# Performance work log

Measured on AMD Instinct MI355X. Metric: run time of the kernel, lower is better.

The kernel has to match this reference:

```python
import jax, jax.numpy as jnp
import numpy as np

B, D, L, E, R = 16384, 2048, 3, 8, 64


def setup_inputs() -> dict:
    key = jax.random.key(0)
    k1, k2, k3, k4 = jax.random.split(key, 4)
    scale = 1.0 / np.sqrt(D)  # ~ PyTorch Linear default init scale
    X0 = jax.random.normal(k1, (B, D), dtype=jnp.float32)
    U = jax.random.normal(k2, (L, E, R, D), dtype=jnp.float32) * scale
    V = jax.random.normal(k3, (L, E, R, D), dtype=jnp.float32) * scale
    Wg = jax.random.normal(k4, (L, E, D), dtype=jnp.float32) * scale
    bg = jnp.zeros((L, E), dtype=jnp.float32)
    return {"X0": X0, "U": U, "V": V, "Wg": Wg, "bg": bg}


def reference(X0, U, V, Wg, bg):
    # X0: (B, D); U, V: (L, E, R, D); Wg: (L, E, D); bg: (L, E)
    Xi = X0
    num_layers = U.shape[0]
    for l in range(num_layers):  # small fixed layer count
        gate = jax.nn.softmax(jnp.einsum('bd,ed->be', Xi, Wg[l]) + bg[l], axis=1)  # (B, E)
        Uo = jnp.einsum('bd,erd->ber', Xi, U[l])  # (B, E, R)
        Vo = jnp.einsum('bd,erd->ber', Xi, V[l])  # (B, E, R)
        expert_out = jnp.sum(Uo * Vo, axis=2)     # (B, E) low-rank bilinear forms
        xw = jnp.sum(expert_out * gate, axis=1, keepdims=True)  # (B, 1)
        Xi = Xi + X0 * xw  # residual cross update (dropout=0, eval mode)
    return Xi
```

## Files before the change

### kernel.cpp

```cpp
#include <hip/hip_runtime.h>
#include <hip/hip_bf16.h>

#define BDIM 16384
#define DDIM 2048
#define LNUM 3
#define ENUM 8
#define NP 24

#define BM 256
#define BK 32

typedef _Float16 f16x8 __attribute__((ext_vector_type(8)));
typedef _Float16 f16x4 __attribute__((ext_vector_type(4)));
typedef float f32x4 __attribute__((ext_vector_type(4)));

__global__ void cvt_w_kernel(const float* __restrict__ U, const float* __restrict__ V,
                             _Float16* __restrict__ Wh) {
    size_t f = (size_t)blockIdx.x * blockDim.x + threadIdx.x;
    size_t elem = f * 4;
    int d   = (int)(elem & (DDIM - 1));
    int row = (int)((elem >> 11) & 127);
    int p   = (int)(elem >> 18);
    const float* src = (row < 64)
        ? (U + ((size_t)(p * 64 + row) * DDIM + d))
        : (V + ((size_t)(p * 64 + (row - 64)) * DDIM + d));
    float4 v = *(const float4*)src;
    f16x4 h = { (_Float16)v.x, (_Float16)v.y, (_Float16)v.z, (_Float16)v.w };
    ((f16x4*)Wh)[f] = h;
}

__global__ __launch_bounds__(256, 4) void gate_kernel(
    const float* __restrict__ X0, const float* __restrict__ Wg,
    float* __restrict__ G, _Float16* __restrict__ X0h) {
    __shared__ float Wgs[NP * 256];
    const int tid = (int)threadIdx.x;
    const int rq  = tid >> 3;
    const int q   = tid & 7;
    const int r0  = blockIdx.x * 64 + rq;
    const int r1  = r0 + 32;

    float acc[2][NP];
#pragma unroll
    for (int r = 0; r < 2; ++r)
#pragma unroll
        for (int j = 0; j < NP; ++j) acc[r][j] = 0.f;

    const float4* x0p = (const float4*)(X0 + (size_t)r0 * DDIM);
    const float4* x1p = (const float4*)(X0 + (size_t)r1 * DDIM);
    f16x4* h0p = (f16x4*)(X0h + (size_t)r0 * DDIM);
    f16x4* h1p = (f16x4*)(X0h + (size_t)r1 * DDIM);

    for (int k0 = 0; k0 < DDIM; k0 += 256) {
        __syncthreads();
#pragma unroll
        for (int t = tid; t < NP * 64; t += 256)
            ((float4*)Wgs)[t] =
                ((const float4*)Wg)[(size_t)(t >> 6) * (DDIM / 4) + (k0 >> 2) + (t & 63)];
        __syncthreads();
#pragma unroll 2
        for (int i = 0; i < 8; ++i) {
            int f4 = i * 8 + q;
            int gc = (k0 >> 2) + f4;
            float4 x0 = x0p[gc];
            float4 x1 = x1p[gc];
            f16x4 h0 = { (_Float16)x0.x, (_Float16)x0.y, (_Float16)x0.z, (_Float16)x0.w };
            f16x4 h1 = { (_Float16)x1.x, (_Float16)x1.y, (_Float16)x1.z, (_Float16)x1.w };
            h0p[gc] = h0;
            h1p[gc] = h1;
#pragma unroll
            for (int j = 0; j < NP; ++j) {
                float4 w = ((const float4*)(Wgs + j * 256))[f4];
                acc[0][j] += x0.x * w.x + x0.y * w.y + x0.z * w.z + x0.w * w.w;
                acc[1][j] += x1.x * w.x + x1.y * w.y + x1.z * w.z + x1.w * w.w;
            }
        }
    }
#pragma unroll
    for (int r = 0; r < 2; ++r)
#pragma unroll
        for (int j = 0; j < NP; ++j) {
            float v = acc[r][j];
            v += __shfl_xor(v, 1);
            v += __shfl_xor(v, 2);
            v += __shfl_xor(v, 4);
            if (q == 0) G[(size_t)j * BDIM + (r == 0 ? r0 : r1)] = v;
        }
}

__global__ __launch_bounds__(256, 2) void gemm_t_kernel(
    const _Float16* __restrict__ Ah,
    const _Float16* __restrict__ Bh,
    float* __restrict__ T)
{
    const int p    = blockIdx.y;
    const int m0   = blockIdx.x * BM;
    const int tid  = (int)threadIdx.x;
    const int wave = tid >> 6;
    const int lane = tid & 63;
    const int mlane = lane & 15;
    const int quad  = lane >> 4;

    __shared__ _Float16 As[BM * BK];
    __shared__ _Float16 Bs[128 * BK];

    const _Float16* Bp = Bh + (size_t)p * 128 * DDIM;

    f32x4 acc[4][8];
#pragma unroll
    for (int i = 0; i < 4; ++i)
#pragma unroll
        for (int j = 0; j < 8; ++j) acc[i][j] = (f32x4){0.f, 0.f, 0.f, 0.f};

    const int srow = lane >> 2;
    const int scol = ((lane & 3) ^ ((lane >> 3) & 3)) * 8;
    const int sw   = (mlane >> 1) & 3;

    for (int k0 = 0; k0 < DDIM; k0 += BK) {
        __syncthreads();
#pragma unroll
        for (int q = 0; q < 4; ++q) {
            int r16 = wave * 64 + q * 16;
            const _Float16* ga = Ah + (size_t)(m0 + r16 + srow) * DDIM + k0 + scol;
            __builtin_amdgcn_global_load_lds(
                (const __attribute__((address_space(1))) void*)ga,
                (__attribute__((address_space(3))) void*)&As[r16 * BK], 16, 0, 0);
        }
#pragma unroll
        for (int q = 0; q < 2; ++q) {
            int r16 = wave * 32 + q * 16;
            const _Float16* gb = Bp + (size_t)(r16 + srow) * DDIM + k0 + scol;
            __builtin_amdgcn_global_load_lds(
                (const __attribute__((address_space(1))) void*)gb,
                (__attribute__((address_space(3))) void*)&Bs[r16 * BK], 16, 0, 0);
        }
        __syncthreads();

        f16x8 aF[4], bF[8];
#pragma unroll
        for (int mi = 0; mi < 4; ++mi)
            aF[mi] = *(const f16x8*)&As[(wave * 64 + mi * 16 + mlane) * BK + ((quad ^ sw) * 8)];
#pragma unroll
        for (int ni = 0; ni < 8; ++ni)
            bF[ni] = *(const f16x8*)&Bs[(ni * 16 + mlane) * BK + ((quad ^ sw) * 8)];
#pragma unroll
        for (int mi = 0; mi < 4; ++mi)
#pragma unroll
            for (int ni = 0; ni < 8; ++ni)
                acc[mi][ni] = __builtin_amdgcn_mfma_f32_16x16x32_f16(
                    aF[mi], bF[ni], acc[mi][ni], 0, 0, 0);
    }

#pragma unroll
    for (int mi = 0; mi < 4; ++mi) {
#pragma unroll
        for (int j = 0; j < 4; ++j) {
            float tp = 0.f;
#pragma unroll
            for (int ni = 0; ni < 4; ++ni)
                tp += acc[mi][ni][j] * acc[mi][ni + 4][j];
            tp += __shfl_xor(tp, 1);
            tp += __shfl_xor(tp, 2);
            tp += __shfl_xor(tp, 4);
            tp += __shfl_xor(tp, 8);
            if (mlane == 0) {
                int m = wave * 64 + mi * 16 + quad * 4 + j;
                T[(size_t)p * BDIM + (m0 + m)] = tp;
            }
        }
    }
}

__global__ void epilogue_kernel(const _Float16* __restrict__ X0h,
                                const float* __restrict__ T,
                                const float* __restrict__ G,
                                const float* __restrict__ bg,
                                float* __restrict__ out) {
    __shared__ float s_sh[16];
    const int b0 = blockIdx.x * 16;
    const int tid = (int)threadIdx.x;
    if (tid < 16) {
        int b = b0 + tid;
        float s = 1.f;
#pragma unroll
        for (int l = 0; l < LNUM; ++l) {
            float logit[ENUM];
            float mx = -1e30f;
#pragma unroll
            for (int e = 0; e < ENUM; ++e) {
                int j = l * ENUM + e;
                float g = s * G[(size_t)j * BDIM + b] + bg[j];
                logit[e] = g;
                mx = fmaxf(mx, g);
            }
            float den = 0.f, num = 0.f;
            float s2 = s * s;
#pragma unroll
            for (int e = 0; e < ENUM; ++e) {
                int j = l * ENUM + e;
                float w = __expf(logit[e] - mx);
                den += w;
                num += w * (s2 * T[(size_t)j * BDIM + b]);
            }
            s += num / den;
        }
        s_sh[tid] = s;
    }
    __syncthreads();
    const int nf4 = DDIM / 4;
    for (int idx = tid; idx < 16 * nf4; idx += 256) {
        int r = idx >> 9;
        int c = idx & (nf4 - 1);
        float s = s_sh[r];
        f16x4 h = ((const f16x4*)(X0h + (size_t)(b0 + r) * DDIM))[c];
        float4 x = { s * (float)h[0], s * (float)h[1], s * (float)h[2], s * (float)h[3] };
        ((float4*)(out + (size_t)(b0 + r) * DDIM))[c] = x;
    }
}

extern "C" void kernel_launch(void* const* d_in, const int* in_sizes, int n_in,
                              void* d_out, int out_size, void* d_ws, size_t ws_size,
                              hipStream_t stream) {
    const float* X0 = (const float*)d_in[0];
    const float* U  = (const float*)d_in[1];
    const float* V  = (const float*)d_in[2];
    const float* Wg = (const float*)d_in[3];
    const float* bg = (const float*)d_in[4];
    float* out = (float*)d_out;

    char* ws = (char*)d_ws;
    _Float16* X0h = (_Float16*)ws;
    _Float16* Wh  = (_Float16*)(ws + 67108864ull);
    float* T      = (float*)(ws + 67108864ull + 12582912ull);
    float* G      = (float*)(ws + 67108864ull + 12582912ull + 1572864ull);

    cvt_w_kernel<<<dim3((NP * 128 * DDIM / 4) / 256), dim3(256), 0, stream>>>(U, V, Wh);
    gate_kernel<<<dim3(BDIM / 64), dim3(256), 0, stream>>>(X0, Wg, G, X0h);
    gemm_t_kernel<<<dim3(BDIM / BM, NP), dim3(256), 0, stream>>>(X0h, Wh, T);
    epilogue_kernel<<<dim3(BDIM / 16), dim3(256), 0, stream>>>(X0h, T, G, bg, out);
}
```

Before: 537.1 us.

## Fold gate projection into the fp16 MFMA GEMM as an extra grid slice

Replaces the scalar fp32 gate kernel, which both converted X0 to fp16 and computed the 24 gate logits with FMAs, with a plain conversion kernel plus a 25th blockIdx.y slice of the MFMA GEMM. That slice multiplies the fp16 X0 by an fp16 copy of Wg and writes the gate logits directly. The aim is to remove the slow scalar dot-product pass in favour of tensor-core work that reuses the existing GEMM tiling. In exchange, gate logits are now computed in fp16 rather than fp32, the gate slice spends MFMA work on padded columns (rows past 24 are loads of duplicated rows), and two extra small kernel launches are added.

Result: faster. 524.1 us (-2.4%).

```diff
diff --git a/kernel.cpp b/kernel.cpp
--- a/kernel.cpp
+++ b/kernel.cpp
@@ -6,6 +6,7 @@
 #define LNUM 3
 #define ENUM 8
 #define NP 24
+#define NPG 25
 
 #define BM 256
 #define BK 32
@@ -29,68 +30,26 @@
     ((f16x4*)Wh)[f] = h;
 }
 
-__global__ __launch_bounds__(256, 4) void gate_kernel(
-    const float* __restrict__ X0, const float* __restrict__ Wg,
-    float* __restrict__ G, _Float16* __restrict__ X0h) {
-    __shared__ float Wgs[NP * 256];
-    const int tid = (int)threadIdx.x;
-    const int rq  = tid >> 3;
-    const int q   = tid & 7;
-    const int r0  = blockIdx.x * 64 + rq;
-    const int r1  = r0 + 32;
-
-    float acc[2][NP];
-#pragma unroll
-    for (int r = 0; r < 2; ++r)
-#pragma unroll
-        for (int j = 0; j < NP; ++j) acc[r][j] = 0.f;
-
-    const float4* x0p = (const float4*)(X0 + (size_t)r0 * DDIM);
-    const float4* x1p = (const float4*)(X0 + (size_t)r1 * DDIM);
-    f16x4* h0p = (f16x4*)(X0h + (size_t)r0 * DDIM);
-    f16x4* h1p = (f16x4*)(X0h + (size_t)r1 * DDIM);
-
-    for (int k0 = 0; k0 < DDIM; k0 += 256) {
-        __syncthreads();
-#pragma unroll
-        for (int t = tid; t < NP * 64; t += 256)
-            ((float4*)Wgs)[t] =
-                ((const float4*)Wg)[(size_t)(t >> 6) * (DDIM / 4) + (k0 >> 2) + (t & 63)];
-        __syncthreads();
-#pragma unroll 2
-        for (int i = 0; i < 8; ++i) {
-            int f4 = i * 8 + q;
-            int gc = (k0 >> 2) + f4;
-            float4 x0 = x0p[gc];
-            float4 x1 = x1p[gc];
-            f16x4 h0 = { (_Float16)x0.x, (_Float16)x0.y, (_Float16)x0.z, (_Float16)x0.w };
-            f16x4 h1 = { (_Float16)x1.x, (_Float16)x1.y, (_Float16)x1.z, (_Float16)x1.w };
-            h0p[gc] = h0;
-            h1p[gc] = h1;
-#pragma unroll
-            for (int j = 0; j < NP; ++j) {
-                float4 w = ((const float4*)(Wgs + j * 256))[f4];
-                acc[0][j] += x0.x * w.x + x0.y * w.y + x0.z * w.z + x0.w * w.w;
-                acc[1][j] += x1.x * w.x + x1.y * w.y + x1.z * w.z + x1.w * w.w;
-            }
-        }
-    }
-#pragma unroll
-    for (int r = 0; r < 2; ++r)
-#pragma unroll
-        for (int j = 0; j < NP; ++j) {
-            float v = acc[r][j];
-            v += __shfl_xor(v, 1);
-            v += __shfl_xor(v, 2);
-            v += __shfl_xor(v, 4);
-            if (q == 0) G[(size_t)j * BDIM + (r == 0 ? r0 : r1)] = v;
-        }
+__global__ void cvt_wg_kernel(const float* __restrict__ Wg, _Float16* __restrict__ Wgh) {
+    int f = (int)(blockIdx.x * blockDim.x + threadIdx.x);
+    float4 v = ((const float4*)Wg)[f];
+    f16x4 h = { (_Float16)v.x, (_Float16)v.y, (_Float16)v.z, (_Float16)v.w };
+    ((f16x4*)Wgh)[f] = h;
+}
+
+__global__ void cvt_x_kernel(const float* __restrict__ X0, _Float16* __restrict__ X0h) {
+    size_t f = (size_t)blockIdx.x * blockDim.x + threadIdx.x;
+    float4 v = ((const float4*)X0)[f];
+    f16x4 h = { (_Float16)v.x, (_Float16)v.y, (_Float16)v.z, (_Float16)v.w };
+    ((f16x4*)X0h)[f] = h;
 }
 
 __global__ __launch_bounds__(256, 2) void gemm_t_kernel(
     const _Float16* __restrict__ Ah,
     const _Float16* __restrict__ Bh,
-    float* __restrict__ T)
+    const _Float16* __restrict__ Wgh,
+    float* __restrict__ T,
+    float* __restrict__ G)
 {
     const int p    = blockIdx.y;
     const int m0   = blockIdx.x * BM;
@@ -103,8 +62,6 @@
     __shared__ _Float16 As[BM * BK];
     __shared__ _Float16 Bs[128 * BK];
 
-    const _Float16* Bp = Bh + (size_t)p * 128 * DDIM;
-
     f32x4 acc[4][8];
 #pragma unroll
     for (int i = 0; i < 4; ++i)
@@ -114,6 +71,9 @@
     const int srow = lane >> 2;
     const int scol = ((lane & 3) ^ ((lane >> 3) & 3)) * 8;
     const int sw   = (mlane >> 1) & 3;
+
+    const bool gate = (p == NP);
+    const _Float16* Bp = gate ? Wgh : (Bh + (size_t)p * 128 * DDIM);
 
     for (int k0 = 0; k0 < DDIM; k0 += BK) {
         __syncthreads();
@@ -128,7 +88,9 @@
 #pragma unroll
         for (int q = 0; q < 2; ++q) {
             int r16 = wave * 32 + q * 16;
-            const _Float16* gb = Bp + (size_t)(r16 + srow) * DDIM + k0 + scol;
+            int r   = r16 + srow;
+            int rb  = (gate && r >= NP) ? (r & 15) : r;
+            const _Float16* gb = Bp + (size_t)rb * DDIM + k0 + scol;
             __builtin_amdgcn_global_load_lds(
                 (const __attribute__((address_space(1))) void*)gb,
                 (__attribute__((address_space(3))) void*)&Bs[r16 * BK], 16, 0, 0);
@@ -150,23 +112,39 @@
                     aF[mi], bF[ni], acc[mi][ni], 0, 0, 0);
     }
 
-#pragma unroll
-    for (int mi = 0; mi < 4; ++mi) {
-#pragma unroll
-        for (int j = 0; j < 4; ++j) {
-            float tp = 0.f;
-#pragma unroll
-            for (int ni = 0; ni < 4; ++ni)
-                tp += acc[mi][ni][j] * acc[mi][ni + 4][j];
-            tp += __shfl_xor(tp, 1);
-            tp += __shfl_xor(tp, 2);
-            tp += __shfl_xor(tp, 4);
-            tp += __shfl_xor(tp, 8);
-            if (mlane == 0) {
-                int m = wave * 64 + mi * 16 + quad * 4 + j;
-                T[(size_t)p * BDIM + (m0 + m)] = tp;
-            }
-        }
+    if (!gate) {
+#pragma unroll
+        for (int mi = 0; mi < 4; ++mi) {
+#pragma unroll
+            for (int j = 0; j < 4; ++j) {
+                float tp = 0.f;
+#pragma unroll
+                for (int ni = 0; ni < 4; ++ni)
+                    tp += acc[mi][ni][j] * acc[mi][ni + 4][j];
+                tp += __shfl_xor(tp, 1);
+                tp += __shfl_xor(tp, 2);
+                tp += __shfl_xor(tp, 4);
+                tp += __shfl_xor(tp, 8);
+                if (mlane == 0) {
+                    int m = wave * 64 + mi * 16 + quad * 4 + j;
+                    T[(size_t)p * BDIM + (m0 + m)] = tp;
+                }
+            }
+        }
+    } else {
+#pragma unroll
+        for (int mi = 0; mi < 4; ++mi)
+#pragma unroll
+            for (int ni = 0; ni < 2; ++ni) {
+                int col = ni * 16 + mlane;
+                if (col < NP) {
+#pragma unroll
+                    for (int j = 0; j < 4; ++j) {
+                        int m = wave * 64 + mi * 16 + quad * 4 + j;
+                        G[(size_t)col * BDIM + (m0 + m)] = acc[mi][ni][j];
+                    }
+                }
+            }
     }
 }
 
@@ -230,11 +208,13 @@
     char* ws = (char*)d_ws;
     _Float16* X0h = (_Float16*)ws;
     _Float16* Wh  = (_Float16*)(ws + 67108864ull);
-    float* T      = (float*)(ws + 67108864ull + 12582912ull);
-    float* G      = (float*)(ws + 67108864ull + 12582912ull + 1572864ull);
+    _Float16* Wgh = (_Float16*)(ws + 79691776ull);
+    float* T      = (float*)(ws + 79790080ull);
+    float* G      = (float*)(ws + 81362944ull);
 
     cvt_w_kernel<<<dim3((NP * 128 * DDIM / 4) / 256), dim3(256), 0, stream>>>(U, V, Wh);
-    gate_kernel<<<dim3(BDIM / 64), dim3(256), 0, stream>>>(X0, Wg, G, X0h);
-    gemm_t_kernel<<<dim3(BDIM / BM, NP), dim3(256), 0, stream>>>(X0h, Wh, T);
+    cvt_wg_kernel<<<dim3((NP * DDIM / 4) / 256), dim3(256), 0, stream>>>(Wg, Wgh);
+    cvt_x_kernel<<<dim3((BDIM * DDIM / 4) / 256), dim3(256), 0, stream>>>(X0, X0h);
+    gemm_t_kernel<<<dim3(BDIM / BM, NPG), dim3(256), 0, stream>>>(X0h, Wh, Wgh, T, G);
     epilogue_kernel<<<dim3(BDIM / 16), dim3(256), 0, stream>>>(X0h, T, G, bg, out);
 }
```
